# Kernel optimization log

Hardware: AMD Instinct MI355X
Metric: run time of the kernel (lower is better)

The kernel has to match this reference:

```python
import jax, jax.numpy as jnp
import numpy as np

MARGIN = 1.0


def setup_inputs() -> dict:
    key = jax.random.key(0)
    k1, k2 = jax.random.split(key)
    B, D, C = 8192, 128, 128
    embeddings = jax.random.normal(k1, (B, D), dtype=jnp.float32)
    labels = jax.random.randint(k2, (B,), 0, C, dtype=jnp.int64)
    return {"embeddings": embeddings, "labels": labels}


def _pairwise_dist(x):
    # Euclidean cdist with a sqrt-safe-at-zero formulation (diag is exactly 0).
    sq = jnp.sum(x * x, axis=-1)
    d2 = jnp.maximum(sq[:, None] + sq[None, :] - 2.0 * (x @ x.T), 0.0)
    pos = d2 > 0
    return jnp.where(pos, jnp.sqrt(jnp.where(pos, d2, 1.0)), 0.0)


def reference(embeddings, labels):
    B = embeddings.shape[0]
    dist = _pairwise_dist(embeddings)  # [B, B]
    same = labels[:, None] == labels[None, :]  # [B, B]
    eye = jnp.eye(B, dtype=bool)
    is_pos = same & ~eye
    is_neg = ~same
    neg_inf = jnp.float32(-jnp.inf)
    pos_inf = jnp.float32(jnp.inf)
    hardest_pos = jnp.max(jnp.where(is_pos, dist, neg_inf), axis=1)  # [B]
    hardest_neg = jnp.min(jnp.where(is_neg, dist, pos_inf), axis=1)  # [B]
    valid = jnp.any(is_pos, axis=1) & jnp.any(is_neg, axis=1)
    per_row = jax.nn.relu(hardest_pos - hardest_neg + MARGIN)
    n_valid = jnp.sum(valid)
    loss = jnp.sum(jnp.where(valid, per_row, 0.0)) / jnp.maximum(n_valid, 1).astype(embeddings.dtype)
    # matches torch fallback of 0.0 when no valid anchors exist
    return jnp.where(n_valid > 0, loss, jnp.float32(0.0))
```

## Files before the change

### kernel.cpp

```cpp
#include <hip/hip_runtime.h>
#include <hip/hip_bf16.h>

typedef __attribute__((ext_vector_type(8))) short short8;
typedef __attribute__((ext_vector_type(4))) float floatx4;

#define B_ROWS 8192
#define DIM    128
#define NSPLIT 16
#define JSPAN  (B_ROWS / NSPLIT)
#define NTILE  (JSPAN / 16)
#define WAVES  4
#define RPW    32
#define BM     (WAVES * RPW)
#define NRB    (B_ROWS / BM)
#define BIAS   4096.0f


#define OFF_SQ   (2u << 20)
#define OFF_D2P  (OFF_SQ + (64u << 10))
#define OFF_D2N  (OFF_D2P + (512u << 10))
#define OFF_ACC  (OFF_D2N + (512u << 10))

__global__ __launch_bounds__(256) void prep_kernel(const float* __restrict__ x,
                                                   __hip_bfloat16* __restrict__ xf,
                                                   float* __restrict__ sq,
                                                   float* __restrict__ acc_sum,
                                                   int* __restrict__ done) {
    if (blockIdx.x == 0 && threadIdx.x == 0) { acc_sum[0] = 0.f; done[0] = 0; }
    const int row  = blockIdx.x * 4 + (threadIdx.x >> 6);
    const int lane = threadIdx.x & 63;
    const float2 v = *reinterpret_cast<const float2*>(x + row * DIM + lane * 2);
    __hip_bfloat162 b2;
    b2.x = __float2bfloat16(v.x);
    b2.y = __float2bfloat16(v.y);
    const int kk = lane >> 4;
    const int g  = (lane >> 2) & 3;
    const int e  = (lane & 3) * 2;
    const int idx = (row >> 4) * 2048 + kk * 512 + (g * 16 + (row & 15)) * 8 + e;
    *reinterpret_cast<__hip_bfloat162*>(xf + idx) = b2;
    float s = v.x * v.x + v.y * v.y;
    #pragma unroll
    for (int m = 1; m < 64; m <<= 1) s += __shfl_xor(s, m, 64);
    if (lane == 0) sq[row] = s;
}

__global__ __launch_bounds__(256, 4) void main_kernel(
    const __hip_bfloat16* __restrict__ xf,
    const float* __restrict__ sq,
    const int*  __restrict__ lab,
    float* __restrict__ d2p,
    float* __restrict__ d2n) {
    const int tid  = threadIdx.x;
    const int lane = tid & 63;
    const int wave = tid >> 6;
    const int l15  = lane & 15;
    const int g    = lane >> 4;
    const int rowbase = blockIdx.x * BM + wave * RPW;
    const int split   = blockIdx.y;
    const int jstart  = split * JSPAN;

    short8 a0[4], a1[4];
    {
        const __hip_bfloat16* ap = xf + (size_t)(rowbase >> 4) * 2048 + lane * 8;
        #pragma unroll
        for (int kk = 0; kk < 4; ++kk) {
            a0[kk] = *reinterpret_cast<const short8*>(ap + kk * 512);
            a1[kk] = *reinterpret_cast<const short8*>(ap + 2048 + kk * 512);
        }
    }
    int labi0[4], labi1[4];
    #pragma unroll
    for (int q = 0; q < 4; ++q) {
        labi0[q] = lab[rowbase + g * 4 + q];
        labi1[q] = lab[rowbase + 16 + g * 4 + q];
    }

    float mx0[4], mn0[4], mx1[4], mn1[4];
    #pragma unroll
    for (int q = 0; q < 4; ++q) {
        mx0[q] = -INFINITY; mx1[q] = -INFINITY;
        mn0[q] =  INFINITY; mn1[q] =  INFINITY;
    }

    const __hip_bfloat16* bbase = xf + (size_t)(jstart >> 4) * 2048 + lane * 8;

    short8 bA[4], bB[4];
    float sqA, sqB; int labA, labB;
    #pragma unroll
    for (int kk = 0; kk < 4; ++kk)
        bA[kk] = *reinterpret_cast<const short8*>(bbase + kk * 512);
    sqA  = sq[jstart + l15];
    labA = lab[jstart + l15];

    #define COMPUTE(bb, sqj, labj)                                              \
    do {                                                                        \
        floatx4 acc0 = {0.f, 0.f, 0.f, 0.f}, acc1 = {0.f, 0.f, 0.f, 0.f};       \
        _Pragma("unroll")                                                       \
        for (int kk = 0; kk < 4; ++kk) {                                        \
            acc0 = __builtin_amdgcn_mfma_f32_16x16x32_bf16(a0[kk], bb[kk], acc0, 0, 0, 0); \
            acc1 = __builtin_amdgcn_mfma_f32_16x16x32_bf16(a1[kk], bb[kk], acc1, 0, 0, 0); \
        }                                                                       \
        const float sqjb = (sqj) + BIAS;                                        \
        _Pragma("unroll")                                                       \
        for (int q = 0; q < 4; ++q) {                                           \
            const float t0 = fmaf(-2.f, acc0[q], ((labj) == labi0[q]) ? sqjb : (sqj)); \
            mx0[q] = fmaxf(mx0[q], t0);                                         \
            mn0[q] = fminf(mn0[q], t0);                                         \
            const float t1 = fmaf(-2.f, acc1[q], ((labj) == labi1[q]) ? sqjb : (sqj)); \
            mx1[q] = fmaxf(mx1[q], t1);                                         \
            mn1[q] = fminf(mn1[q], t1);                                         \
        }                                                                       \
    } while (0)

    for (int jt = 0; jt < NTILE; jt += 2) {
        {
            const __hip_bfloat16* bp = bbase + (size_t)(jt + 1) * 2048;
            #pragma unroll
            for (int kk = 0; kk < 4; ++kk)
                bB[kk] = *reinterpret_cast<const short8*>(bp + kk * 512);
            sqB  = sq[jstart + (jt + 1) * 16 + l15];
            labB = lab[jstart + (jt + 1) * 16 + l15];
        }
        COMPUTE(bA, sqA, labA);
        if (jt + 2 < NTILE) {
            const __hip_bfloat16* bp = bbase + (size_t)(jt + 2) * 2048;
            #pragma unroll
            for (int kk = 0; kk < 4; ++kk)
                bA[kk] = *reinterpret_cast<const short8*>(bp + kk * 512);
            sqA  = sq[jstart + (jt + 2) * 16 + l15];
            labA = lab[jstart + (jt + 2) * 16 + l15];
        }
        COMPUTE(bB, sqB, labB);
    }
    #undef COMPUTE

    #pragma unroll
    for (int q = 0; q < 4; ++q) {
        #pragma unroll
        for (int mk = 1; mk < 16; mk <<= 1) {
            mx0[q] = fmaxf(mx0[q], __shfl_xor(mx0[q], mk, 64));
            mn0[q] = fminf(mn0[q], __shfl_xor(mn0[q], mk, 64));
            mx1[q] = fmaxf(mx1[q], __shfl_xor(mx1[q], mk, 64));
            mn1[q] = fminf(mn1[q], __shfl_xor(mn1[q], mk, 64));
        }
    }
    if (l15 == 0) {
        #pragma unroll
        for (int q = 0; q < 4; ++q) {
            const int i0 = rowbase + g * 4 + q;
            const int i1 = rowbase + 16 + g * 4 + q;
            d2p[split * B_ROWS + i0] = sq[i0] + (mx0[q] - BIAS);
            d2n[split * B_ROWS + i0] = sq[i0] + mn0[q];
            d2p[split * B_ROWS + i1] = sq[i1] + (mx1[q] - BIAS);
            d2n[split * B_ROWS + i1] = sq[i1] + mn1[q];
        }
    }
}

__global__ __launch_bounds__(256) void combine_kernel(
    const float* __restrict__ d2p, const float* __restrict__ d2n,
    float* __restrict__ acc_sum, int* __restrict__ done,
    float* __restrict__ out) {
    const int row = blockIdx.x * 256 + threadIdx.x;
    float p = -INFINITY, n = INFINITY;
    #pragma unroll
    for (int s = 0; s < NSPLIT; ++s) {
        p = fmaxf(p, d2p[s * B_ROWS + row]);
        n = fminf(n, d2n[s * B_ROWS + row]);
    }
    float v = fmaxf(sqrtf(fmaxf(p, 0.f)) - sqrtf(fmaxf(n, 0.f)) + 1.0f, 0.f);
    #pragma unroll
    for (int mk = 1; mk < 64; mk <<= 1) v += __shfl_xor(v, mk, 64);
    __shared__ float sv[4];
    const int wv = threadIdx.x >> 6;
    if ((threadIdx.x & 63) == 0) sv[wv] = v;
    __syncthreads();
    if (threadIdx.x == 0) {
        atomicAdd(acc_sum, sv[0] + sv[1] + sv[2] + sv[3]);
        __threadfence();
        const int old = atomicAdd(done, 1);
        if (old == (int)gridDim.x - 1) {
            const float fs = atomicAdd(acc_sum, 0.f);
            out[0] = fs / (float)B_ROWS;
        }
    }
}

extern "C" void kernel_launch(void* const* d_in, const int* in_sizes, int n_in,
                              void* d_out, int out_size, void* d_ws, size_t ws_size,
                              hipStream_t stream) {
    const float* x   = (const float*)d_in[0];
    const int*   lab = (const int*)d_in[1];
    float*       out = (float*)d_out;

    char* ws = (char*)d_ws;
    __hip_bfloat16* xf = (__hip_bfloat16*)ws;
    float* sq      = (float*)(ws + OFF_SQ);
    float* d2p     = (float*)(ws + OFF_D2P);
    float* d2n     = (float*)(ws + OFF_D2N);
    float* acc_sum = (float*)(ws + OFF_ACC);
    int*   done    = (int*)(ws + OFF_ACC + 4);

    prep_kernel<<<B_ROWS / 4, 256, 0, stream>>>(x, xf, sq, acc_sum, done);
    main_kernel<<<dim3(NRB, NSPLIT), 256, 0, stream>>>(xf, sq, lab, d2p, d2n);
    combine_kernel<<<B_ROWS / 256, 256, 0, stream>>>(d2p, d2n, acc_sum, done, out);
}
```

Baseline: 38.27 us.

## Double rows per wave and restructure B-tile pipeline with batched min/max

Each wave now covers 64 rows (four 16-row MFMA sub-tiles) instead of 32, so every loaded B tile feeds twice as many MFMAs and the number of row blocks is halved. The B-tile prefetch is reorganized so both ping-pong buffers are loaded ahead, and the min/max reduction is deferred until after both tiles' MFMAs are done. The intent is less global/L2 B traffic per FLOP and more independent MFMA work in flight. The cost is higher register pressure, with launch bounds lowered to 2 blocks/SM, and only 32x16 = 512 blocks in the grid.

```diff
diff --git a/kernel.cpp b/kernel.cpp
--- a/kernel.cpp
+++ b/kernel.cpp
@@ -10,7 +10,7 @@
 #define JSPAN  (B_ROWS / NSPLIT)
 #define NTILE  (JSPAN / 16)
 #define WAVES  4
-#define RPW    32
+#define RPW    64
 #define BM     (WAVES * RPW)
 #define NRB    (B_ROWS / BM)
 #define BIAS   4096.0f
@@ -44,7 +44,7 @@
     if (lane == 0) sq[row] = s;
 }
 
-__global__ __launch_bounds__(256, 4) void main_kernel(
+__global__ __launch_bounds__(256, 2) void main_kernel(
     const __hip_bfloat16* __restrict__ xf,
     const float* __restrict__ sq,
     const int*  __restrict__ lab,
@@ -59,69 +59,63 @@
     const int split   = blockIdx.y;
     const int jstart  = split * JSPAN;
 
-    short8 a0[4], a1[4];
-    {
-        const __hip_bfloat16* ap = xf + (size_t)(rowbase >> 4) * 2048 + lane * 8;
-        #pragma unroll
-        for (int kk = 0; kk < 4; ++kk) {
-            a0[kk] = *reinterpret_cast<const short8*>(ap + kk * 512);
-            a1[kk] = *reinterpret_cast<const short8*>(ap + 2048 + kk * 512);
-        }
-    }
-    int labi0[4], labi1[4];
-    #pragma unroll
-    for (int q = 0; q < 4; ++q) {
-        labi0[q] = lab[rowbase + g * 4 + q];
-        labi1[q] = lab[rowbase + 16 + g * 4 + q];
-    }
-
-    float mx0[4], mn0[4], mx1[4], mn1[4];
-    #pragma unroll
-    for (int q = 0; q < 4; ++q) {
-        mx0[q] = -INFINITY; mx1[q] = -INFINITY;
-        mn0[q] =  INFINITY; mn1[q] =  INFINITY;
-    }
+    short8 a[4][4];
+    #pragma unroll
+    for (int s = 0; s < 4; ++s) {
+        const __hip_bfloat16* ap = xf + ((size_t)(rowbase >> 4) + s) * 2048 + lane * 8;
+        #pragma unroll
+        for (int kk = 0; kk < 4; ++kk)
+            a[s][kk] = *reinterpret_cast<const short8*>(ap + kk * 512);
+    }
+    int labi[4][4];
+    #pragma unroll
+    for (int s = 0; s < 4; ++s)
+        #pragma unroll
+        for (int q = 0; q < 4; ++q)
+            labi[s][q] = lab[rowbase + s * 16 + g * 4 + q];
+
+    float mx[4][4], mn[4][4];
+    #pragma unroll
+    for (int s = 0; s < 4; ++s)
+        #pragma unroll
+        for (int q = 0; q < 4; ++q) { mx[s][q] = -INFINITY; mn[s][q] = INFINITY; }
 
     const __hip_bfloat16* bbase = xf + (size_t)(jstart >> 4) * 2048 + lane * 8;
 
     short8 bA[4], bB[4];
     float sqA, sqB; int labA, labB;
     #pragma unroll
-    for (int kk = 0; kk < 4; ++kk)
+    for (int kk = 0; kk < 4; ++kk) {
         bA[kk] = *reinterpret_cast<const short8*>(bbase + kk * 512);
-    sqA  = sq[jstart + l15];
-    labA = lab[jstart + l15];
-
-    #define COMPUTE(bb, sqj, labj)                                              \
+        bB[kk] = *reinterpret_cast<const short8*>(bbase + 2048 + kk * 512);
+    }
+    sqA  = sq[jstart + l15];          labA = lab[jstart + l15];
+    sqB  = sq[jstart + 16 + l15];     labB = lab[jstart + 16 + l15];
+
+    float tA[4][4], tB[4][4];
+
+    #define MFMA_TILE(BB, T, SQJ, LABJ)                                         \
     do {                                                                        \
-        floatx4 acc0 = {0.f, 0.f, 0.f, 0.f}, acc1 = {0.f, 0.f, 0.f, 0.f};       \
+        floatx4 acc[4];                                                         \
+        _Pragma("unroll")                                                       \
+        for (int s = 0; s < 4; ++s) acc[s] = (floatx4){0.f, 0.f, 0.f, 0.f};     \
         _Pragma("unroll")                                                       \
         for (int kk = 0; kk < 4; ++kk) {                                        \
-            acc0 = __builtin_amdgcn_mfma_f32_16x16x32_bf16(a0[kk], bb[kk], acc0, 0, 0, 0); \
-            acc1 = __builtin_amdgcn_mfma_f32_16x16x32_bf16(a1[kk], bb[kk], acc1, 0, 0, 0); \
+            _Pragma("unroll")                                                   \
+            for (int s = 0; s < 4; ++s)                                         \
+                acc[s] = __builtin_amdgcn_mfma_f32_16x16x32_bf16(a[s][kk], BB[kk], acc[s], 0, 0, 0); \
         }                                                                       \
-        const float sqjb = (sqj) + BIAS;                                        \
+        const float sqjb = (SQJ) + BIAS;                                        \
         _Pragma("unroll")                                                       \
-        for (int q = 0; q < 4; ++q) {                                           \
-            const float t0 = fmaf(-2.f, acc0[q], ((labj) == labi0[q]) ? sqjb : (sqj)); \
-            mx0[q] = fmaxf(mx0[q], t0);                                         \
-            mn0[q] = fminf(mn0[q], t0);                                         \
-            const float t1 = fmaf(-2.f, acc1[q], ((labj) == labi1[q]) ? sqjb : (sqj)); \
-            mx1[q] = fmaxf(mx1[q], t1);                                         \
-            mn1[q] = fminf(mn1[q], t1);                                         \
+        for (int s = 0; s < 4; ++s) {                                           \
+            _Pragma("unroll")                                                   \
+            for (int q = 0; q < 4; ++q)                                         \
+                T[s][q] = fmaf(-2.f, acc[s][q], ((LABJ) == labi[s][q]) ? sqjb : (SQJ)); \
         }                                                                       \
     } while (0)
 
     for (int jt = 0; jt < NTILE; jt += 2) {
-        {
-            const __hip_bfloat16* bp = bbase + (size_t)(jt + 1) * 2048;
-            #pragma unroll
-            for (int kk = 0; kk < 4; ++kk)
-                bB[kk] = *reinterpret_cast<const short8*>(bp + kk * 512);
-            sqB  = sq[jstart + (jt + 1) * 16 + l15];
-            labB = lab[jstart + (jt + 1) * 16 + l15];
-        }
-        COMPUTE(bA, sqA, labA);
+        MFMA_TILE(bA, tA, sqA, labA);
         if (jt + 2 < NTILE) {
             const __hip_bfloat16* bp = bbase + (size_t)(jt + 2) * 2048;
             #pragma unroll
@@ -130,30 +124,45 @@
             sqA  = sq[jstart + (jt + 2) * 16 + l15];
             labA = lab[jstart + (jt + 2) * 16 + l15];
         }
-        COMPUTE(bB, sqB, labB);
-    }
-    #undef COMPUTE
-
-    #pragma unroll
-    for (int q = 0; q < 4; ++q) {
-        #pragma unroll
-        for (int mk = 1; mk < 16; mk <<= 1) {
-            mx0[q] = fmaxf(mx0[q], __shfl_xor(mx0[q], mk, 64));
-            mn0[q] = fminf(mn0[q], __shfl_xor(mn0[q], mk, 64));
-            mx1[q] = fmaxf(mx1[q], __shfl_xor(mx1[q], mk, 64));
-            mn1[q] = fminf(mn1[q], __shfl_xor(mn1[q], mk, 64));
-        }
-    }
+        MFMA_TILE(bB, tB, sqB, labB);
+        if (jt + 3 < NTILE) {
+            const __hip_bfloat16* bp = bbase + (size_t)(jt + 3) * 2048;
+            #pragma unroll
+            for (int kk = 0; kk < 4; ++kk)
+                bB[kk] = *reinterpret_cast<const short8*>(bp + kk * 512);
+            sqB  = sq[jstart + (jt + 3) * 16 + l15];
+            labB = lab[jstart + (jt + 3) * 16 + l15];
+        }
+        #pragma unroll
+        for (int s = 0; s < 4; ++s)
+            #pragma unroll
+            for (int q = 0; q < 4; ++q) {
+                mx[s][q] = fmaxf(fmaxf(mx[s][q], tA[s][q]), tB[s][q]);
+                mn[s][q] = fminf(fminf(mn[s][q], tA[s][q]), tB[s][q]);
+            }
+    }
+    #undef MFMA_TILE
+
+    #pragma unroll
+    for (int s = 0; s < 4; ++s)
+        #pragma unroll
+        for (int q = 0; q < 4; ++q) {
+            #pragma unroll
+            for (int mk = 1; mk < 16; mk <<= 1) {
+                mx[s][q] = fmaxf(mx[s][q], __shfl_xor(mx[s][q], mk, 64));
+                mn[s][q] = fminf(mn[s][q], __shfl_xor(mn[s][q], mk, 64));
+            }
+        }
     if (l15 == 0) {
         #pragma unroll
-        for (int q = 0; q < 4; ++q) {
-            const int i0 = rowbase + g * 4 + q;
-            const int i1 = rowbase + 16 + g * 4 + q;
-            d2p[split * B_ROWS + i0] = sq[i0] + (mx0[q] - BIAS);
-            d2n[split * B_ROWS + i0] = sq[i0] + mn0[q];
-            d2p[split * B_ROWS + i1] = sq[i1] + (mx1[q] - BIAS);
-            d2n[split * B_ROWS + i1] = sq[i1] + mn1[q];
-        }
+        for (int s = 0; s < 4; ++s)
+            #pragma unroll
+            for (int q = 0; q < 4; ++q) {
+                const int i = rowbase + s * 16 + g * 4 + q;
+                const float sqi = sq[i];
+                d2p[split * B_ROWS + i] = sqi + (mx[s][q] - BIAS);
+                d2n[split * B_ROWS + i] = sqi + mn[s][q];
+            }
     }
 }
 
```

After: 34.66 us. 9.4% less time.
